# Performance work log

Hardware: AMD Instinct MI355X
Metric: run time of the kernel (lower is better)

## Reference

```python
import jax, jax.numpy as jnp
import numpy as np

EPS = 1e-5  # torch BatchNorm default eps
B, C, T, NOUT, NCLS = 4096, 32, 512, 16, 4


def setup_inputs() -> dict:
    key = jax.random.key(0)
    ks = jax.random.split(key, 12)
    s = lambda k, shape: jax.random.normal(k, shape, jnp.float32) * 0.05
    return {
        "de": jax.random.normal(ks[0], (B, C, T), jnp.float32),
        "adj": jax.random.normal(ks[1], (B, C, C), jnp.float32),  # unused by forward (module recomputes corr)
        "dw_w": s(ks[2], (C, 1, 3)),      # depthwise Conv1d weight [C,1,3]
        "dw_b": s(ks[3], (C,)),
        "pw_w": s(ks[4], (C, C)),          # pointwise 1x1 conv [out,in]
        "pw_b": s(ks[5], (C,)),
        "bn1_g": jnp.ones((C,), jnp.float32),
        "bn1_b": jnp.zeros((C,), jnp.float32),
        "gc_w": s(ks[6], (T, NOUT)),       # GraphConvolution weight
        "fc_w": s(ks[7], (C * NOUT, C)),   # fc62 Linear(512,32)
        "fc_b": s(ks[8], (C,)),
        "bn2_g": jnp.ones((C,), jnp.float32),
        "bn2_b": jnp.zeros((C,), jnp.float32),
        "cls_w": s(ks[9], (C, NCLS)),      # fcclass Linear(32,4)
        "cls_b": s(ks[10], (NCLS,)),
    }


def reference(de, adj, dw_w, dw_b, pw_w, pw_b, bn1_g, bn1_b, gc_w,
              fc_w, fc_b, bn2_g, bn2_b, cls_w, cls_b):
    # --- SeparableConv2d (really 1d): depthwise k=3 -> pointwise 1x1 -> BN -> relu ---
    x = jax.lax.conv_general_dilated(
        de, dw_w, window_strides=(1,), padding=[(1, 1)],
        dimension_numbers=("NCH", "OIH", "NCH"),
        feature_group_count=de.shape[1]) + dw_b[None, :, None]
    x = jnp.einsum("oc,bct->bot", pw_w, x) + pw_b[None, :, None]
    m = x.mean((0, 2), keepdims=True)
    v = x.var((0, 2), keepdims=True)  # biased, as BN normalization uses
    x = (x - m) / jnp.sqrt(v + EPS) * bn1_g[None, :, None] + bn1_b[None, :, None]
    x = jax.nn.relu(x)                       # [B, C, T]

    # --- batched Pearson corrcoef over the time axis (vectorizes the per-sample loop) ---
    xt = x.transpose(0, 2, 1)                # [B, T, C]
    Tn = xt.shape[1]
    f = (Tn - 1) / Tn
    xc = xt - xt.mean(1, keepdims=True)
    num = jnp.einsum("btn,btm->bnm", xc, xc) / Tn   # biased covariance
    var = xt.var(1, ddof=1)                         # torch var default unbiased
    den = jnp.sqrt(var[:, :, None] * var[:, None, :]) * f
    cor = num / den                          # [B, C, C]

    # --- Chebyshev graph convolution (single K term, adj = cor) + relu ---
    g = jnp.einsum("bnm,bmt->bnt", cor, x)   # message passing over channel graph
    g = jax.nn.relu(jnp.einsum("bnt,to->bno", g, gc_w))  # [B, C, 16]

    # --- fc62: Linear -> BN1d -> (dropout: identity) -> sigmoid ---
    h = g.reshape(g.shape[0], -1) @ fc_w + fc_b          # [B, 32]
    m2 = h.mean(0)
    v2 = h.var(0)
    h = (h - m2) / jnp.sqrt(v2 + EPS) * bn2_g + bn2_b
    h = jax.nn.sigmoid(h)

    return h @ cls_w + cls_b                 # [B, 4]
```

## Files before the change

### kernel.cpp

```cpp
#include <hip/hip_runtime.h>
#include <math.h>

#define BB 4096
#define CC 32
#define TT 512
#define NOUTC 16
#define EPSF 1e-5f
#define XS 520


typedef __attribute__((ext_vector_type(16))) float f32x16;
typedef __attribute__((ext_vector_type(4)))  float f32x4;
typedef __attribute__((ext_vector_type(8)))  short short8;
typedef __attribute__((ext_vector_type(4)))  unsigned int u32x4;
typedef __attribute__((ext_vector_type(4)))  float vf4;
typedef vf4 __attribute__((aligned(4))) vf4u;

__device__ __forceinline__ unsigned short f2b(float f) {
  unsigned int u = __builtin_bit_cast(unsigned int, f);
  return (unsigned short)((u + 0x7FFFu + ((u >> 16) & 1u)) >> 16);
}
__device__ __forceinline__ float blo(unsigned int u) {
  return __builtin_bit_cast(float, u << 16);
}
__device__ __forceinline__ float bhi(unsigned int u) {
  return __builtin_bit_cast(float, u & 0xFFFF0000u);
}

__device__ __forceinline__ void conv_cols(const float* __restrict__ deb,
    const float* __restrict__ dw, const float* __restrict__ db_,
    int tid, float* x1A, float* x1B) {
  int t0 = tid * 2;
  int off = (tid == 0) ? 0 : ((tid == 255) ? t0 - 2 : t0 - 1);
#pragma unroll
  for (int c = 0; c < CC; c++) {
    vf4u v = *reinterpret_cast<const vf4u*>(deb + c * TT + off);
    float vm1 = (tid == 0) ? 0.f : ((tid == 255) ? v.y : v.x);
    float v0  = (tid == 0) ? v.x : ((tid == 255) ? v.z : v.y);
    float vp1 = (tid == 0) ? v.y : ((tid == 255) ? v.w : v.z);
    float vp2 = (tid == 0) ? v.z : ((tid == 255) ? 0.f : v.w);
    float w0 = dw[c * 3], w1 = dw[c * 3 + 1], w2 = dw[c * 3 + 2], bc = db_[c];
    x1A[c] = fmaf(w0, vm1, fmaf(w1, v0, fmaf(w2, vp1, bc)));
    x1B[c] = fmaf(w0, v0, fmaf(w1, vp1, fmaf(w2, vp2, bc)));
  }
}

__global__ __launch_bounds__(256) void k1_stats(const float* __restrict__ de,
    const float* __restrict__ dw, const float* __restrict__ db_,
    const float* __restrict__ pw, const float* __restrict__ pwb,
    float* __restrict__ part, unsigned int* __restrict__ x2h, int useWs) {
  __shared__ float pr[4 * 64];
  int tid = threadIdx.x, b = blockIdx.x;
  int w = tid >> 6, lane = tid & 63;
  const float* deb = de + (size_t)b * CC * TT;
  float x1A[CC], x1B[CC];
  conv_cols(deb, dw, db_, tid, x1A, x1B);
  unsigned int* xw = x2h + (size_t)b * CC * 256;
#pragma unroll
  for (int o = 0; o < CC; o++) {
    float aA = pwb[o], aB = pwb[o];
#pragma unroll
    for (int c = 0; c < CC; c++) { float pv = pw[o * CC + c]; aA = fmaf(pv, x1A[c], aA); aB = fmaf(pv, x1B[c], aB); }
    if (useWs) xw[o * 256 + tid] = (unsigned int)f2b(aA) | ((unsigned int)f2b(aB) << 16);
    float s = aA + aB, q = fmaf(aA, aA, aB * aB);
#pragma unroll
    for (int d = 1; d < 64; d <<= 1) { s += __shfl_xor(s, d); q += __shfl_xor(q, d); }
    if (lane == 0) { pr[w * 64 + o] = s; pr[w * 64 + 32 + o] = q; }
  }
  __syncthreads();
  if (tid < 64) {
    part[(size_t)tid * BB + b] = pr[tid] + pr[64 + tid] + pr[128 + tid] + pr[192 + tid];
  }
}

__global__ void k2_bn1(const float* __restrict__ part, const float* __restrict__ g,
                       const float* __restrict__ bta, float* __restrict__ ws) {
  __shared__ float redS[256], redQ[256];
  int o = blockIdx.x, tid = threadIdx.x;
  const float* ps = part + (size_t)o * BB;
  const float* pq = part + (size_t)(CC + o) * BB;
  float s = 0, q = 0;
  for (int i = tid; i < BB; i += 256) { s += ps[i]; q += pq[i]; }
  redS[tid] = s; redQ[tid] = q;
  __syncthreads();
  for (int k = 128; k > 0; k >>= 1) {
    if (tid < k) { redS[tid] += redS[tid + k]; redQ[tid] += redQ[tid + k]; }
    __syncthreads();
  }
  if (tid == 0) {
    float N = (float)BB * (float)TT;
    float mean = redS[0] / N;
    float var = redQ[0] / N - mean * mean;
    float sc = g[o] / sqrtf(var + EPSF);
    ws[o] = sc;
    ws[32 + o] = bta[o] - mean * sc;
  }
}

__global__ __launch_bounds__(256) void k3_main(const float* __restrict__ de,
    const float* __restrict__ dw, const float* __restrict__ db_,
    const float* __restrict__ pw, const float* __restrict__ pwb,
    const float* __restrict__ ws, const float* __restrict__ gcw,
    const float* __restrict__ fcw, const float* __restrict__ fcb,
    float* __restrict__ hT, const unsigned int* __restrict__ x2h, int useWs) {
  __shared__ __align__(16) unsigned short x_s[CC * XS];
  __shared__ __align__(16) unsigned short gc_s[NOUTC * XS];
  __shared__ float gramP[2][CC * CC];
  __shared__ float zP[2][CC * NOUTC];
  __shared__ float num_s[CC * 33];
  __shared__ float red16[CC * 8];
  __shared__ float mu_s[CC], inv_s[CC];
  __shared__ float Zi_s[CC * NOUTC];
  __shared__ float g2_s[CC * NOUTC];
  __shared__ float red2[CC * 9];

  int tid = threadIdx.x, b = blockIdx.x;
  int w = tid >> 6, lane = tid & 63;
  int t0 = tid * 2;

  for (int i = tid; i < TT * NOUTC; i += 256) {
    int t = i >> 4, o = i & 15;
    gc_s[o * XS + t] = f2b(gcw[i]);
  }

  if (useWs) {
    const unsigned int* xr = x2h + (size_t)b * CC * 256;
#pragma unroll
    for (int o = 0; o < CC; o++) {
      unsigned int u = xr[o * 256 + tid];
      float sc = ws[o], sh = ws[32 + o];
      unsigned short hA = f2b(fmaxf(fmaf(blo(u), sc, sh), 0.f));
      unsigned short hB = f2b(fmaxf(fmaf(bhi(u), sc, sh), 0.f));
      *(unsigned int*)(&x_s[o * XS + t0]) = (unsigned int)hA | ((unsigned int)hB << 16);
    }
  } else {
    const float* deb = de + (size_t)b * CC * TT;
    float x1A[CC], x1B[CC];
    conv_cols(deb, dw, db_, tid, x1A, x1B);
#pragma unroll
    for (int o = 0; o < CC; o++) {
      float aA = pwb[o], aB = pwb[o];
#pragma unroll
      for (int c = 0; c < CC; c++) { float pv = pw[o * CC + c]; aA = fmaf(pv, x1A[c], aA); aB = fmaf(pv, x1B[c], aB); }
      float sc = ws[o], sh = ws[32 + o];
      unsigned short hA = f2b(fmaxf(fmaf(aA, sc, sh), 0.f));
      unsigned short hB = f2b(fmaxf(fmaf(aB, sc, sh), 0.f));
      *(unsigned int*)(&x_s[o * XS + t0]) = (unsigned int)hA | ((unsigned int)hB << 16);
    }
  }
  __syncthreads();

  {
    int c = tid >> 3, j = tid & 7;
    float s = 0.f;
#pragma unroll
    for (int it = 0; it < 8; it++) {
      u32x4 u = *reinterpret_cast<const u32x4*>(&x_s[c * XS + j * 64 + it * 8]);
#pragma unroll
      for (int k = 0; k < 4; k++) s += blo(u[k]) + bhi(u[k]);
    }
    red16[c * 8 + j] = s;
  }

  if (w < 2) {
    int m = lane & 31, kh = lane >> 5;
    f32x16 acc;
#pragma unroll
    for (int r = 0; r < 16; r++) acc[r] = 0.f;
    int kbase = w * 256 + kh * 8;
#pragma unroll
    for (int kk = 0; kk < 256; kk += 16) {
      short8 a = *(const short8*)(&x_s[m * XS + kbase + kk]);
      acc = __builtin_amdgcn_mfma_f32_32x32x16_bf16(a, a, acc, 0, 0, 0);
    }
#pragma unroll
    for (int r = 0; r < 16; r++) {
      int row = (r & 3) + 8 * (r >> 2) + 4 * kh;
      gramP[w][row * CC + m] = acc[r];
    }
  } else {
    int w2 = w - 2;
    int n16 = lane & 15, q = lane >> 4;
    f32x4 ac0, ac1;
#pragma unroll
    for (int r = 0; r < 4; r++) { ac0[r] = 0.f; ac1[r] = 0.f; }
    int kbase = w2 * 256 + q * 8;
#pragma unroll
    for (int kk = 0; kk < 256; kk += 32) {
      short8 bfr = *(const short8*)(&gc_s[n16 * XS + kbase + kk]);
      short8 af0 = *(const short8*)(&x_s[n16 * XS + kbase + kk]);
      short8 af1 = *(const short8*)(&x_s[(16 + n16) * XS + kbase + kk]);
      ac0 = __builtin_amdgcn_mfma_f32_16x16x32_bf16(af0, bfr, ac0, 0, 0, 0);
      ac1 = __builtin_amdgcn_mfma_f32_16x16x32_bf16(af1, bfr, ac1, 0, 0, 0);
    }
#pragma unroll
    for (int r = 0; r < 4; r++) {
      int row = q * 4 + r;
      zP[w2][row * NOUTC + n16] = ac0[r];
      zP[w2][(16 + row) * NOUTC + n16] = ac1[r];
    }
  }
  __syncthreads();
  if (tid < CC) {
    float s = 0.f;
#pragma unroll
    for (int j = 0; j < 8; j++) s += red16[tid * 8 + j];
    mu_s[tid] = s;
  }
  __syncthreads();
  for (int i = tid; i < CC * CC; i += 256) {
    int n = i >> 5, m = i & 31;
    num_s[n * 33 + m] = gramP[0][i] + gramP[1][i] - mu_s[n] * mu_s[m] * (1.f / (float)TT);
  }
  for (int i = tid; i < CC * NOUTC; i += 256) Zi_s[i] = zP[0][i] + zP[1][i];
  __syncthreads();
  if (tid < CC) inv_s[tid] = rsqrtf(num_s[tid * 33 + tid]);
  __syncthreads();
  for (int i = tid; i < CC * NOUTC; i += 256) {
    int n = i >> 4, o = i & 15;
    float s = 0.f;
#pragma unroll
    for (int m = 0; m < CC; m++) s = fmaf(num_s[n * 33 + m] * inv_s[m], Zi_s[m * NOUTC + o], s);
    g2_s[i] = fmaxf(s * inv_s[n], 0.f);
  }
  __syncthreads();
  {
    int j = tid & 31, ch = tid >> 5;
    float p = 0.f;
#pragma unroll
    for (int ii = 0; ii < 64; ii++) {
      int i = ch * 64 + ii;
      p = fmaf(g2_s[i], fcw[i * CC + j], p);
    }
    red2[j * 9 + ch] = p;
  }
  __syncthreads();
  if (tid < CC) {
    float h = fcb[tid];
#pragma unroll
    for (int ch = 0; ch < 8; ch++) h += red2[tid * 9 + ch];
    hT[(size_t)tid * BB + b] = h;
  }
}

__global__ void k4_bn2(const float* __restrict__ hT, const float* __restrict__ g,
                       const float* __restrict__ bta, float* __restrict__ ws) {
  __shared__ float redS[256], redQ[256];
  int j = blockIdx.x, tid = threadIdx.x;
  const float* row = hT + (size_t)j * BB;
  float s = 0, q = 0;
  for (int i = tid; i < BB; i += 256) { float v = row[i]; s += v; q = fmaf(v, v, q); }
  redS[tid] = s; redQ[tid] = q;
  __syncthreads();
  for (int k = 128; k > 0; k >>= 1) {
    if (tid < k) { redS[tid] += redS[tid + k]; redQ[tid] += redQ[tid + k]; }
    __syncthreads();
  }
  if (tid == 0) {
    float N = (float)BB;
    float mean = redS[0] / N;
    float var = redQ[0] / N - mean * mean;
    float sc = g[j] / sqrtf(var + EPSF);
    ws[64 + j] = sc;
    ws[96 + j] = bta[j] - mean * sc;
  }
}

__global__ void k5_out(const float* __restrict__ hT, const float* __restrict__ ws,
                       const float* __restrict__ clsw, const float* __restrict__ clsb,
                       float* __restrict__ out) {
  __shared__ float hs[CC * 257];
  int b0 = blockIdx.x * 256, tid = threadIdx.x;
  for (int i = tid; i < CC * 256; i += 256) {
    int j = i >> 8, bb = i & 255;
    float v = fmaf(hT[(size_t)j * BB + b0 + bb], ws[64 + j], ws[96 + j]);
    hs[j * 257 + bb] = 1.f / (1.f + expf(-v));
  }
  __syncthreads();
  float o0 = clsb[0], o1 = clsb[1], o2 = clsb[2], o3 = clsb[3];
#pragma unroll
  for (int j = 0; j < CC; j++) {
    float h = hs[j * 257 + tid];
    o0 = fmaf(h, clsw[j * 4 + 0], o0);
    o1 = fmaf(h, clsw[j * 4 + 1], o1);
    o2 = fmaf(h, clsw[j * 4 + 2], o2);
    o3 = fmaf(h, clsw[j * 4 + 3], o3);
  }
  float4* out4 = reinterpret_cast<float4*>(out);
  out4[b0 + tid] = make_float4(o0, o1, o2, o3);
}

extern "C" void kernel_launch(void* const* d_in, const int* in_sizes, int n_in,
                              void* d_out, int out_size, void* d_ws, size_t ws_size,
                              hipStream_t stream) {
  const float* de   = (const float*)d_in[0];
  const float* dw   = (const float*)d_in[2];
  const float* db_  = (const float*)d_in[3];
  const float* pw   = (const float*)d_in[4];
  const float* pwb  = (const float*)d_in[5];
  const float* bn1g = (const float*)d_in[6];
  const float* bn1b = (const float*)d_in[7];
  const float* gcw  = (const float*)d_in[8];
  const float* fcw  = (const float*)d_in[9];
  const float* fcb  = (const float*)d_in[10];
  const float* bn2g = (const float*)d_in[11];
  const float* bn2b = (const float*)d_in[12];
  const float* clsw = (const float*)d_in[13];
  const float* clsb = (const float*)d_in[14];

  float* ws   = (float*)d_ws;
  float* hT   = ws + 128;
  float* part = ws + 131200;
  unsigned int* x2h = (unsigned int*)(ws + 393344);
  float* out  = (float*)d_out;

  size_t need = 393344ull * 4ull + (size_t)BB * CC * 256 * 4;
  int useWs = (ws_size >= need) ? 1 : 0;

  k1_stats<<<BB, 256, 0, stream>>>(de, dw, db_, pw, pwb, part, x2h, useWs);
  k2_bn1<<<CC, 256, 0, stream>>>(part, bn1g, bn1b, ws);
  k3_main<<<BB, 256, 0, stream>>>(de, dw, db_, pw, pwb, ws, gcw, fcw, fcb, hT, x2h, useWs);
  k4_bn2<<<CC, 256, 0, stream>>>(hT, bn2g, bn2b, ws);
  k5_out<<<BB / 256, 256, 0, stream>>>(hT, ws, clsw, clsb, out);
}
```

Before: 512.0 us.

## Derive BN1 stats from depthwise Gram and move pointwise conv to MFMA

The first pass now computes only the depthwise conv output and its per-sample 32x32 Gram matrix and channel sums on MFMA. BN1 mean and variance come from these through the pointwise weights, so the pointwise conv is no longer run in the stats pass and the bf16 intermediate is no longer written and re-read. The main kernel recomputes the depthwise conv and does the pointwise conv as a bf16 MFMA, with the weights split into hi and lo bf16 parts for accuracy. This trades the extra global traffic for recomputation and a larger reduction over 1056 partial values per sample. Computing variance as E[x²] minus mean² from bf16 Gram sums risks precision loss.

```diff
diff --git a/kernel.cpp b/kernel.cpp
--- a/kernel.cpp
+++ b/kernel.cpp
@@ -7,12 +7,14 @@
 #define NOUTC 16
 #define EPSF 1e-5f
 #define XS 520
+#define XST 40
 
 
 typedef __attribute__((ext_vector_type(16))) float f32x16;
 typedef __attribute__((ext_vector_type(4)))  float f32x4;
 typedef __attribute__((ext_vector_type(8)))  short short8;
 typedef __attribute__((ext_vector_type(4)))  unsigned int u32x4;
+typedef __attribute__((ext_vector_type(2)))  unsigned int u32x2;
 typedef __attribute__((ext_vector_type(4)))  float vf4;
 typedef vf4 __attribute__((aligned(4))) vf4u;
 
@@ -20,6 +22,9 @@
   unsigned int u = __builtin_bit_cast(unsigned int, f);
   return (unsigned short)((u + 0x7FFFu + ((u >> 16) & 1u)) >> 16);
 }
+__device__ __forceinline__ float b2f(unsigned short h) {
+  return __builtin_bit_cast(float, ((unsigned int)h) << 16);
+}
 __device__ __forceinline__ float blo(unsigned int u) {
   return __builtin_bit_cast(float, u << 16);
 }
@@ -27,125 +32,216 @@
   return __builtin_bit_cast(float, u & 0xFFFF0000u);
 }
 
-__device__ __forceinline__ void conv_cols(const float* __restrict__ deb,
+__device__ __forceinline__ void conv1(const float* __restrict__ deb,
     const float* __restrict__ dw, const float* __restrict__ db_,
-    int tid, float* x1A, float* x1B) {
-  int t0 = tid * 2;
-  int off = (tid == 0) ? 0 : ((tid == 255) ? t0 - 2 : t0 - 1);
-#pragma unroll
-  for (int c = 0; c < CC; c++) {
-    vf4u v = *reinterpret_cast<const vf4u*>(deb + c * TT + off);
-    float vm1 = (tid == 0) ? 0.f : ((tid == 255) ? v.y : v.x);
-    float v0  = (tid == 0) ? v.x : ((tid == 255) ? v.z : v.y);
-    float vp1 = (tid == 0) ? v.y : ((tid == 255) ? v.w : v.z);
-    float vp2 = (tid == 0) ? v.z : ((tid == 255) ? 0.f : v.w);
-    float w0 = dw[c * 3], w1 = dw[c * 3 + 1], w2 = dw[c * 3 + 2], bc = db_[c];
-    x1A[c] = fmaf(w0, vm1, fmaf(w1, v0, fmaf(w2, vp1, bc)));
-    x1B[c] = fmaf(w0, v0, fmaf(w1, vp1, fmaf(w2, vp2, bc)));
-  }
-}
-
-__global__ __launch_bounds__(256) void k1_stats(const float* __restrict__ de,
+    int c, int off, int tid, float& A, float& Bv) {
+  vf4u v = *reinterpret_cast<const vf4u*>(deb + c * TT + off);
+  float vm1 = (tid == 0) ? 0.f : ((tid == 255) ? v.y : v.x);
+  float v0  = (tid == 0) ? v.x : ((tid == 255) ? v.z : v.y);
+  float vp1 = (tid == 0) ? v.y : ((tid == 255) ? v.w : v.z);
+  float vp2 = (tid == 0) ? v.z : ((tid == 255) ? 0.f : v.w);
+  float w0 = dw[c * 3], w1 = dw[c * 3 + 1], w2 = dw[c * 3 + 2], bc = db_[c];
+  A  = fmaf(w0, vm1, fmaf(w1, v0, fmaf(w2, vp1, bc)));
+  Bv = fmaf(w0, v0, fmaf(w1, vp1, fmaf(w2, vp2, bc)));
+}
+
+__global__ __launch_bounds__(256) void kA_gram(const float* __restrict__ de,
     const float* __restrict__ dw, const float* __restrict__ db_,
-    const float* __restrict__ pw, const float* __restrict__ pwb,
-    float* __restrict__ part, unsigned int* __restrict__ x2h, int useWs) {
-  __shared__ float pr[4 * 64];
+    float* __restrict__ part) {
+  __shared__ __align__(16) unsigned short x_s[CC * XS];
+  __shared__ float gramP[4][CC * CC];
+  __shared__ float red16[CC * 8];
   int tid = threadIdx.x, b = blockIdx.x;
   int w = tid >> 6, lane = tid & 63;
   const float* deb = de + (size_t)b * CC * TT;
-  float x1A[CC], x1B[CC];
-  conv_cols(deb, dw, db_, tid, x1A, x1B);
-  unsigned int* xw = x2h + (size_t)b * CC * 256;
-#pragma unroll
-  for (int o = 0; o < CC; o++) {
-    float aA = pwb[o], aB = pwb[o];
-#pragma unroll
-    for (int c = 0; c < CC; c++) { float pv = pw[o * CC + c]; aA = fmaf(pv, x1A[c], aA); aB = fmaf(pv, x1B[c], aB); }
-    if (useWs) xw[o * 256 + tid] = (unsigned int)f2b(aA) | ((unsigned int)f2b(aB) << 16);
-    float s = aA + aB, q = fmaf(aA, aA, aB * aB);
-#pragma unroll
-    for (int d = 1; d < 64; d <<= 1) { s += __shfl_xor(s, d); q += __shfl_xor(q, d); }
-    if (lane == 0) { pr[w * 64 + o] = s; pr[w * 64 + 32 + o] = q; }
-  }
-  __syncthreads();
-  if (tid < 64) {
-    part[(size_t)tid * BB + b] = pr[tid] + pr[64 + tid] + pr[128 + tid] + pr[192 + tid];
-  }
-}
-
-__global__ void k2_bn1(const float* __restrict__ part, const float* __restrict__ g,
-                       const float* __restrict__ bta, float* __restrict__ ws) {
-  __shared__ float redS[256], redQ[256];
-  int o = blockIdx.x, tid = threadIdx.x;
-  const float* ps = part + (size_t)o * BB;
-  const float* pq = part + (size_t)(CC + o) * BB;
-  float s = 0, q = 0;
-  for (int i = tid; i < BB; i += 256) { s += ps[i]; q += pq[i]; }
-  redS[tid] = s; redQ[tid] = q;
-  __syncthreads();
-  for (int k = 128; k > 0; k >>= 1) {
-    if (tid < k) { redS[tid] += redS[tid + k]; redQ[tid] += redQ[tid + k]; }
-    __syncthreads();
-  }
-  if (tid == 0) {
-    float N = (float)BB * (float)TT;
-    float mean = redS[0] / N;
-    float var = redQ[0] / N - mean * mean;
-    float sc = g[o] / sqrtf(var + EPSF);
-    ws[o] = sc;
-    ws[32 + o] = bta[o] - mean * sc;
-  }
-}
-
-__global__ __launch_bounds__(256) void k3_main(const float* __restrict__ de,
+  int t0 = tid * 2;
+  int off = (tid == 0) ? 0 : ((tid == 255) ? t0 - 2 : t0 - 1);
+  for (int c = 0; c < CC; c++) {
+    float a, bv;
+    conv1(deb, dw, db_, c, off, tid, a, bv);
+    *(unsigned int*)(&x_s[c * XS + t0]) = (unsigned int)f2b(a) | ((unsigned int)f2b(bv) << 16);
+  }
+  __syncthreads();
+  {
+    int c = tid >> 3, j = tid & 7;
+    float s = 0.f;
+#pragma unroll
+    for (int it = 0; it < 8; it++) {
+      u32x4 u = *reinterpret_cast<const u32x4*>(&x_s[c * XS + j * 64 + it * 8]);
+#pragma unroll
+      for (int k = 0; k < 4; k++) s += blo(u[k]) + bhi(u[k]);
+    }
+    red16[c * 8 + j] = s;
+  }
+  {
+    int m = lane & 31, kh = lane >> 5;
+    f32x16 acc;
+#pragma unroll
+    for (int r = 0; r < 16; r++) acc[r] = 0.f;
+    int kbase = w * 128 + kh * 8;
+#pragma unroll
+    for (int kk = 0; kk < 128; kk += 16) {
+      short8 a = *(const short8*)(&x_s[m * XS + kbase + kk]);
+      acc = __builtin_amdgcn_mfma_f32_32x32x16_bf16(a, a, acc, 0, 0, 0);
+    }
+#pragma unroll
+    for (int r = 0; r < 16; r++) {
+      int row = (r & 3) + 8 * (r >> 2) + 4 * kh;
+      gramP[w][row * CC + m] = acc[r];
+    }
+  }
+  __syncthreads();
+  float* pb = part + (size_t)b * 1056;
+  for (int i = tid; i < CC * CC; i += 256)
+    pb[i] = gramP[0][i] + gramP[1][i] + gramP[2][i] + gramP[3][i];
+  if (tid < CC) {
+    float s = 0.f;
+#pragma unroll
+    for (int j = 0; j < 8; j++) s += red16[tid * 8 + j];
+    pb[1024 + tid] = s;
+  }
+}
+
+__global__ __launch_bounds__(256) void k2_reduce(const float* __restrict__ part,
+                                                 float* __restrict__ Gred) {
+  __shared__ float red[8][32];
+  int tid = threadIdx.x;
+  int j = blockIdx.x * 32 + (tid & 31);
+  int sub = tid >> 5;
+  float s = 0.f;
+  if (j < 1056) {
+    for (int bb = sub; bb < BB; bb += 8) s += part[(size_t)bb * 1056 + j];
+  }
+  red[sub][tid & 31] = s;
+  __syncthreads();
+  if (tid < 32 && blockIdx.x * 32 + tid < 1056) {
+    float t = 0.f;
+#pragma unroll
+    for (int k = 0; k < 8; k++) t += red[k][tid];
+    Gred[blockIdx.x * 32 + tid] = t;
+  }
+}
+
+__global__ void k2_stats(const float* __restrict__ Gred,
+                         const float* __restrict__ pw, const float* __restrict__ pwb,
+                         const float* __restrict__ g, const float* __restrict__ bta,
+                         float* __restrict__ ws) {
+  int o = threadIdx.x;
+  if (o >= CC) return;
+  const float* G1 = Gred;
+  const float* s1 = Gred + 1024;
+  float N = (float)BB * (float)TT;
+  float spo = 0.f;
+  for (int c = 0; c < CC; c++) spo = fmaf(pw[o * CC + c], s1[c], spo);
+  float mean = spo / N + pwb[o];
+  float q = 0.f;
+  for (int c = 0; c < CC; c++) {
+    float t = 0.f;
+    for (int c2 = 0; c2 < CC; c2++) t = fmaf(G1[c * CC + c2], pw[o * CC + c2], t);
+    q = fmaf(pw[o * CC + c], t, q);
+  }
+  float msq = q / N + 2.f * pwb[o] * (spo / N) + pwb[o] * pwb[o];
+  float var = msq - mean * mean;
+  float sc = g[o] / sqrtf(var + EPSF);
+  ws[o] = sc;
+  ws[32 + o] = bta[o] - mean * sc;
+}
+
+__global__ __launch_bounds__(256) void kC_main(const float* __restrict__ de,
     const float* __restrict__ dw, const float* __restrict__ db_,
-    const float* __restrict__ pw, const float* __restrict__ pwb,
-    const float* __restrict__ ws, const float* __restrict__ gcw,
-    const float* __restrict__ fcw, const float* __restrict__ fcb,
-    float* __restrict__ hT, const unsigned int* __restrict__ x2h, int useWs) {
-  __shared__ __align__(16) unsigned short x_s[CC * XS];
+    const float* __restrict__ pw, const float* __restrict__ ws,
+    const float* __restrict__ gcw, const float* __restrict__ fcw,
+    const float* __restrict__ fcb, float* __restrict__ hT,
+    const float* __restrict__ pwb) {
+  __shared__ __align__(16) unsigned short bufA[TT * XST];
   __shared__ __align__(16) unsigned short gc_s[NOUTC * XS];
+  __shared__ __align__(16) unsigned short pwh_s[CC * CC];
+  __shared__ __align__(16) unsigned short pwl_s[CC * CC];
+  __shared__ float sc_s[CC], sh_s[CC];
   __shared__ float gramP[2][CC * CC];
   __shared__ float zP[2][CC * NOUTC];
   __shared__ float num_s[CC * 33];
   __shared__ float red16[CC * 8];
   __shared__ float mu_s[CC], inv_s[CC];
-  __shared__ float Zi_s[CC * NOUTC];
-  __shared__ float g2_s[CC * NOUTC];
-  __shared__ float red2[CC * 9];
-
-  int tid = threadIdx.x, b = blockIdx.x;
+
+  int tid = threadIdx.x;
+  int b = BB - 1 - blockIdx.x;
   int w = tid >> 6, lane = tid & 63;
-  int t0 = tid * 2;
+  const float* deb = de + (size_t)b * CC * TT;
 
   for (int i = tid; i < TT * NOUTC; i += 256) {
     int t = i >> 4, o = i & 15;
     gc_s[o * XS + t] = f2b(gcw[i]);
   }
-
-  if (useWs) {
-    const unsigned int* xr = x2h + (size_t)b * CC * 256;
-#pragma unroll
-    for (int o = 0; o < CC; o++) {
-      unsigned int u = xr[o * 256 + tid];
-      float sc = ws[o], sh = ws[32 + o];
-      unsigned short hA = f2b(fmaxf(fmaf(blo(u), sc, sh), 0.f));
-      unsigned short hB = f2b(fmaxf(fmaf(bhi(u), sc, sh), 0.f));
-      *(unsigned int*)(&x_s[o * XS + t0]) = (unsigned int)hA | ((unsigned int)hB << 16);
-    }
-  } else {
-    const float* deb = de + (size_t)b * CC * TT;
-    float x1A[CC], x1B[CC];
-    conv_cols(deb, dw, db_, tid, x1A, x1B);
-#pragma unroll
-    for (int o = 0; o < CC; o++) {
-      float aA = pwb[o], aB = pwb[o];
-#pragma unroll
-      for (int c = 0; c < CC; c++) { float pv = pw[o * CC + c]; aA = fmaf(pv, x1A[c], aA); aB = fmaf(pv, x1B[c], aB); }
-      float sc = ws[o], sh = ws[32 + o];
-      unsigned short hA = f2b(fmaxf(fmaf(aA, sc, sh), 0.f));
-      unsigned short hB = f2b(fmaxf(fmaf(aB, sc, sh), 0.f));
-      *(unsigned int*)(&x_s[o * XS + t0]) = (unsigned int)hA | ((unsigned int)hB << 16);
+  for (int i = tid; i < CC * CC; i += 256) {
+    float p = pw[i];
+    unsigned short h = f2b(p);
+    pwh_s[i] = h;
+    pwl_s[i] = f2b(p - b2f(h));
+  }
+  if (tid < CC) {
+    float sc = ws[tid];
+    sc_s[tid] = sc;
+    sh_s[tid] = fmaf(sc, pwb[tid], ws[32 + tid]);
+  }
+
+  {
+    int t0 = tid * 2;
+    int off = (tid == 0) ? 0 : ((tid == 255) ? t0 - 2 : t0 - 1);
+#pragma unroll
+    for (int cc = 0; cc < 4; cc++) {
+      unsigned int pa[4], pb[4];
+#pragma unroll
+      for (int k = 0; k < 8; k += 2) {
+        float a0, b0, a1, b1;
+        conv1(deb, dw, db_, cc * 8 + k, off, tid, a0, b0);
+        conv1(deb, dw, db_, cc * 8 + k + 1, off, tid, a1, b1);
+        pa[k >> 1] = (unsigned int)f2b(a0) | ((unsigned int)f2b(a1) << 16);
+        pb[k >> 1] = (unsigned int)f2b(b0) | ((unsigned int)f2b(b1) << 16);
+      }
+      u32x2 wa0 = {pa[0], pa[1]}, wa1 = {pa[2], pa[3]};
+      u32x2 wb0 = {pb[0], pb[1]}, wb1 = {pb[2], pb[3]};
+      *(u32x2*)(&bufA[(size_t)t0 * XST + cc * 8]) = wa0;
+      *(u32x2*)(&bufA[(size_t)t0 * XST + cc * 8 + 4]) = wa1;
+      *(u32x2*)(&bufA[(size_t)(t0 + 1) * XST + cc * 8]) = wb0;
+      *(u32x2*)(&bufA[(size_t)(t0 + 1) * XST + cc * 8 + 4]) = wb1;
+    }
+  }
+  __syncthreads();
+
+  int n16 = lane & 15, q = lane >> 4;
+  int h = w >> 1, ct0 = (w & 1) * 16;
+  f32x4 acc[16];
+#pragma unroll
+  for (int i = 0; i < 16; i++) { acc[i][0] = 0.f; acc[i][1] = 0.f; acc[i][2] = 0.f; acc[i][3] = 0.f; }
+  {
+    short8 ahi = *(const short8*)(&pwh_s[(h * 16 + n16) * CC + q * 8]);
+    short8 alo = *(const short8*)(&pwl_s[(h * 16 + n16) * CC + q * 8]);
+#pragma unroll
+    for (int i = 0; i < 16; i++) {
+      int t = (ct0 + i) * 16 + n16;
+      short8 bx = *(const short8*)(&bufA[(size_t)t * XST + q * 8]);
+      acc[i] = __builtin_amdgcn_mfma_f32_16x16x32_bf16(alo, bx, acc[i], 0, 0, 0);
+      acc[i] = __builtin_amdgcn_mfma_f32_16x16x32_bf16(ahi, bx, acc[i], 0, 0, 0);
+    }
+  }
+  float scr[4], shr[4];
+#pragma unroll
+  for (int r = 0; r < 4; r++) {
+    int o = h * 16 + q * 4 + r;
+    scr[r] = sc_s[o]; shr[r] = sh_s[o];
+  }
+  __syncthreads();
+
+  unsigned short* xsv = bufA;
+#pragma unroll
+  for (int i = 0; i < 16; i++) {
+    int t = (ct0 + i) * 16 + n16;
+#pragma unroll
+    for (int r = 0; r < 4; r++) {
+      int o = h * 16 + q * 4 + r;
+      float val = fmaxf(fmaf(acc[i][r], scr[r], shr[r]), 0.f);
+      xsv[o * XS + t] = f2b(val);
     }
   }
   __syncthreads();
@@ -155,32 +251,30 @@
     float s = 0.f;
 #pragma unroll
     for (int it = 0; it < 8; it++) {
-      u32x4 u = *reinterpret_cast<const u32x4*>(&x_s[c * XS + j * 64 + it * 8]);
+      u32x4 u = *reinterpret_cast<const u32x4*>(&xsv[c * XS + j * 64 + it * 8]);
 #pragma unroll
       for (int k = 0; k < 4; k++) s += blo(u[k]) + bhi(u[k]);
     }
     red16[c * 8 + j] = s;
   }
-
   if (w < 2) {
     int m = lane & 31, kh = lane >> 5;
-    f32x16 acc;
-#pragma unroll
-    for (int r = 0; r < 16; r++) acc[r] = 0.f;
+    f32x16 g16;
+#pragma unroll
+    for (int r = 0; r < 16; r++) g16[r] = 0.f;
     int kbase = w * 256 + kh * 8;
 #pragma unroll
     for (int kk = 0; kk < 256; kk += 16) {
-      short8 a = *(const short8*)(&x_s[m * XS + kbase + kk]);
-      acc = __builtin_amdgcn_mfma_f32_32x32x16_bf16(a, a, acc, 0, 0, 0);
+      short8 a = *(const short8*)(&xsv[m * XS + kbase + kk]);
+      g16 = __builtin_amdgcn_mfma_f32_32x32x16_bf16(a, a, g16, 0, 0, 0);
     }
 #pragma unroll
     for (int r = 0; r < 16; r++) {
       int row = (r & 3) + 8 * (r >> 2) + 4 * kh;
-      gramP[w][row * CC + m] = acc[r];
+      gramP[w][row * CC + m] = g16[r];
     }
   } else {
     int w2 = w - 2;
-    int n16 = lane & 15, q = lane >> 4;
     f32x4 ac0, ac1;
 #pragma unroll
     for (int r = 0; r < 4; r++) { ac0[r] = 0.f; ac1[r] = 0.f; }
@@ -188,8 +282,8 @@
 #pragma unroll
     for (int kk = 0; kk < 256; kk += 32) {
       short8 bfr = *(const short8*)(&gc_s[n16 * XS + kbase + kk]);
-      short8 af0 = *(const short8*)(&x_s[n16 * XS + kbase + kk]);
-      short8 af1 = *(const short8*)(&x_s[(16 + n16) * XS + kbase + kk]);
+      short8 af0 = *(const short8*)(&xsv[n16 * XS + kbase + kk]);
+      short8 af1 = *(const short8*)(&xsv[(16 + n16) * XS + kbase + kk]);
       ac0 = __builtin_amdgcn_mfma_f32_16x16x32_bf16(af0, bfr, ac0, 0, 0, 0);
       ac1 = __builtin_amdgcn_mfma_f32_16x16x32_bf16(af1, bfr, ac1, 0, 0, 0);
     }
@@ -201,6 +295,9 @@
     }
   }
   __syncthreads();
+  float* Zi_s = (float*)bufA;
+  float* g2_s = Zi_s + 512;
+  float* red2 = Zi_s + 1024;
   if (tid < CC) {
     float s = 0.f;
 #pragma unroll
@@ -236,10 +333,10 @@
   }
   __syncthreads();
   if (tid < CC) {
-    float h = fcb[tid];
-#pragma unroll
-    for (int ch = 0; ch < 8; ch++) h += red2[tid * 9 + ch];
-    hT[(size_t)tid * BB + b] = h;
+    float hh = fcb[tid];
+#pragma unroll
+    for (int ch = 0; ch < 8; ch++) hh += red2[tid * 9 + ch];
+    hT[(size_t)tid * BB + b] = hh;
   }
 }
 
@@ -248,9 +345,9 @@
   __shared__ float redS[256], redQ[256];
   int j = blockIdx.x, tid = threadIdx.x;
   const float* row = hT + (size_t)j * BB;
-  float s = 0, q = 0;
-  for (int i = tid; i < BB; i += 256) { float v = row[i]; s += v; q = fmaf(v, v, q); }
-  redS[tid] = s; redQ[tid] = q;
+  float s = 0, qq = 0;
+  for (int i = tid; i < BB; i += 256) { float v = row[i]; s += v; qq = fmaf(v, v, qq); }
+  redS[tid] = s; redQ[tid] = qq;
   __syncthreads();
   for (int k = 128; k > 0; k >>= 1) {
     if (tid < k) { redS[tid] += redS[tid + k]; redQ[tid] += redQ[tid + k]; }
@@ -280,11 +377,11 @@
   float o0 = clsb[0], o1 = clsb[1], o2 = clsb[2], o3 = clsb[3];
 #pragma unroll
   for (int j = 0; j < CC; j++) {
-    float h = hs[j * 257 + tid];
-    o0 = fmaf(h, clsw[j * 4 + 0], o0);
-    o1 = fmaf(h, clsw[j * 4 + 1], o1);
-    o2 = fmaf(h, clsw[j * 4 + 2], o2);
-    o3 = fmaf(h, clsw[j * 4 + 3], o3);
+    float hv = hs[j * 257 + tid];
+    o0 = fmaf(hv, clsw[j * 4 + 0], o0);
+    o1 = fmaf(hv, clsw[j * 4 + 1], o1);
+    o2 = fmaf(hv, clsw[j * 4 + 2], o2);
+    o3 = fmaf(hv, clsw[j * 4 + 3], o3);
   }
   float4* out4 = reinterpret_cast<float4*>(out);
   out4[b0 + tid] = make_float4(o0, o1, o2, o3);
@@ -309,17 +406,15 @@
   const float* clsb = (const float*)d_in[14];
 
   float* ws   = (float*)d_ws;
-  float* hT   = ws + 128;
-  float* part = ws + 131200;
-  unsigned int* x2h = (unsigned int*)(ws + 393344);
+  float* Gred = ws + 128;
+  float* hT   = ws + 2048;
+  float* part = ws + 133120;
   float* out  = (float*)d_out;
 
-  size_t need = 393344ull * 4ull + (size_t)BB * CC * 256 * 4;
-  int useWs = (ws_size >= need) ? 1 : 0;
-
-  k1_stats<<<BB, 256, 0, stream>>>(de, dw, db_, pw, pwb, part, x2h, useWs);
-  k2_bn1<<<CC, 256, 0, stream>>>(part, bn1g, bn1b, ws);
-  k3_main<<<BB, 256, 0, stream>>>(de, dw, db_, pw, pwb, ws, gcw, fcw, fcb, hT, x2h, useWs);
+  kA_gram<<<BB, 256, 0, stream>>>(de, dw, db_, part);
+  k2_reduce<<<33, 256, 0, stream>>>(part, Gred);
+  k2_stats<<<1, 64, 0, stream>>>(Gred, pw, pwb, bn1g, bn1b, ws);
+  kC_main<<<BB, 256, 0, stream>>>(de, dw, db_, pw, ws, gcw, fcw, fcb, hT, pwb);
   k4_bn2<<<CC, 256, 0, stream>>>(hT, bn2g, bn2b, ws);
   k5_out<<<BB / 256, 256, 0, stream>>>(hT, ws, clsw, clsb, out);
 }
```

Result: slower. 664.4 us (+29.8%).
